# Kernel optimization log

Measured on AMD Instinct MI355X. Metric: run time of the kernel, lower is better.

Reference implementation:

```python
import jax, jax.numpy as jnp
import numpy as np

B, S, D, C = 8, 4096, 512, 2048


def setup_inputs() -> dict:
    key = jax.random.key(0)
    kx, kc = jax.random.split(key)
    x = jax.random.normal(kx, (B, S, D), dtype=jnp.float32)
    # kaiming_uniform_(a=sqrt(5)) on a [*,D,C] tensor ~ U(-bound, bound); exact init
    # distribution is irrelevant for the math, so plain scaled uniform is used.
    bound = 1.0 / np.sqrt(D)
    codebook = jax.random.uniform(kc, (1, 1, D, C), dtype=jnp.float32,
                                  minval=-bound, maxval=bound)
    return {"x": x, "codebook": codebook}


def reference(x, codebook):
    # Original: ((x[..., :, None] - codebook) ** 2).mean(dim=-2) -> [B, S, C]
    # Equivalent GEMM form: mean_d(x_d^2) + mean_d(c_dk^2) - (2/D) * x . c_k
    d = x.shape[-1]
    cb = codebook.reshape(codebook.shape[-2], codebook.shape[-1])  # [D, C]
    x2 = jnp.mean(x * x, axis=-1, keepdims=True)                   # [B, S, 1]
    c2 = jnp.mean(cb * cb, axis=0)                                 # [C]
    xc = jnp.einsum('bsd,dc->bsc', x, cb) / d                      # [B, S, C]
    return x2 + c2 - 2.0 * xc
```

## Files before the change

kernel.cpp:

```cpp
#include <hip/hip_runtime.h>
#include <hip/hip_bf16.h>


typedef __attribute__((ext_vector_type(8))) short bf16x8;
typedef __attribute__((ext_vector_type(4))) float f32x4;

#define M_ROWS 32768
#define K_DIM  512
#define N_COLS 2048

__device__ __forceinline__ unsigned short f2bf(float f) {
    unsigned int u = __float_as_uint(f);
    return (unsigned short)((u + 0x7fffu + ((u >> 16) & 1u)) >> 16);
}

__device__ __forceinline__ void gload_lds16(const void* g, void* l) {
    __builtin_amdgcn_global_load_lds(
        (const __attribute__((address_space(1))) unsigned int*)g,
        (__attribute__((address_space(3))) unsigned int*)l,
        16, 0, 0);
}

__global__ __launch_bounds__(256) void prep_x_kernel(const float* __restrict__ x,
                                                     unsigned short* __restrict__ xb,
                                                     float* __restrict__ x2) {
    const int wid = threadIdx.x >> 6;
    const int lane = threadIdx.x & 63;
    const int row = (blockIdx.x << 2) + wid;
    const float4* p4 = reinterpret_cast<const float4*>(x + (size_t)row * K_DIM);
    float4 v0 = p4[lane];
    float4 v1 = p4[lane + 64];
    float ss = v0.x*v0.x + v0.y*v0.y + v0.z*v0.z + v0.w*v0.w
             + v1.x*v1.x + v1.y*v1.y + v1.z*v1.z + v1.w*v1.w;
    union { unsigned short us[4]; uint2 u2; } pa, pb;
    pa.us[0] = f2bf(v0.x); pa.us[1] = f2bf(v0.y); pa.us[2] = f2bf(v0.z); pa.us[3] = f2bf(v0.w);
    pb.us[0] = f2bf(v1.x); pb.us[1] = f2bf(v1.y); pb.us[2] = f2bf(v1.z); pb.us[3] = f2bf(v1.w);
    uint2* dst = reinterpret_cast<uint2*>(xb + (size_t)row * K_DIM);
    dst[lane]      = pa.u2;
    dst[lane + 64] = pb.u2;
    #pragma unroll
    for (int off = 32; off; off >>= 1) ss += __shfl_xor(ss, off);
    if (lane == 0) x2[row] = ss * (1.0f / (float)K_DIM);
}

__global__ __launch_bounds__(256) void prep_cb_kernel(const float* __restrict__ cb,
                                                      unsigned short* __restrict__ cbT) {
    __shared__ float tile[32][65];
    const int k0 = blockIdx.x * 32;
    const int n0 = blockIdx.y * 64;
    const int tx = threadIdx.x & 63;
    const int ty = threadIdx.x >> 6;
    #pragma unroll
    for (int i = 0; i < 8; ++i) {
        const int k = ty + i * 4;
        tile[k][tx] = cb[(size_t)(k0 + k) * N_COLS + n0 + tx];
    }
    __syncthreads();
    const int kc = threadIdx.x & 31;
    const int nr = threadIdx.x >> 5;
    #pragma unroll
    for (int i = 0; i < 8; ++i) {
        const int n = nr + i * 8;
        cbT[(size_t)(n0 + n) * K_DIM + k0 + kc] = f2bf(tile[kc][n] * 0.00390625f);
    }
}

__global__ __launch_bounds__(256) void c2_kernel(const float* __restrict__ cb,
                                                 float* __restrict__ c2) {
    __shared__ float p[4][64];
    const int t = threadIdx.x;
    const int nl = t & 63;
    const int kc = t >> 6;
    const int n = blockIdx.x * 64 + nl;
    float s = 0.0f;
    for (int k = kc * 128; k < kc * 128 + 128; ++k) {
        float v = cb[(size_t)k * N_COLS + n];
        s += v * v;
    }
    p[kc][nl] = s;
    __syncthreads();
    if (t < 64) {
        c2[blockIdx.x * 64 + t] =
            (p[0][t] + p[1][t] + p[2][t] + p[3][t]) * (1.0f / (float)K_DIM);
    }
}


__device__ __forceinline__ bf16x8 frag_ld(const unsigned short* h, int r, int lhi) {
    const int off = r * 32 + ((lhi ^ ((r >> 1) & 3)) << 3);
    return *reinterpret_cast<const bf16x8*>(&h[off]);
}

#define BAR()  do { asm volatile("" ::: "memory"); \
                    __builtin_amdgcn_s_barrier();  \
                    asm volatile("" ::: "memory"); } while (0)
#define GATE_(n) asm volatile("s_waitcnt vmcnt(" #n ")" ::: "memory")
#define GATE(n) GATE_(n)

__global__ __launch_bounds__(512, 4) void gemm_kernel(
        const unsigned short* __restrict__ A,
        const unsigned short* __restrict__ Bt,
        const float* __restrict__ x2,
        const float* __restrict__ c2,
        float* __restrict__ out) {
    __shared__ unsigned short smem[3][12288];

    const int tid  = threadIdx.x;
    const int wid  = tid >> 6;
    const int lane = tid & 63;
    const int wr64 = (wid >> 2) * 64;
    const int wc64 = (wid & 3) * 64;
    const int l15 = lane & 15;
    const int lhi = lane >> 4;

    const int bid  = blockIdx.x;
    const int lbid = (bid & 7) * 256 + (bid >> 3);
    const int m0 = (lbid >> 3) * 128;
    const int n0 = (lbid & 7) * 256;

    const unsigned short* Ab = A  + (size_t)m0 * K_DIM;
    const unsigned short* Bb = Bt + (size_t)n0 * K_DIM;

    const int o16a  = wid * 64 + lane;
    const int rowa  = o16a >> 2;
    const int sla   = (o16a & 3) ^ ((rowa >> 1) & 3);
    const size_t aoff = (size_t)rowa * K_DIM + sla * 8;
    const int o16b0 = wid * 64 + lane;
    const int rowb0 = o16b0 >> 2;
    const size_t boff0 = (size_t)rowb0 * K_DIM + (((o16b0 & 3) ^ ((rowb0 >> 1) & 3)) * 8);
    const int o16b1 = 512 + wid * 64 + lane;
    const int rowb1 = o16b1 >> 2;
    const size_t boff1 = (size_t)rowb1 * K_DIM + (((o16b1 & 3) ^ ((rowb1 >> 1) & 3)) * 8);

    f32x4 acc[4][4] = {};

#define STAGE(KT, BUF)                                                         \
    do {                                                                       \
        gload_lds16(Ab + aoff  + (KT) * 32, &smem[(BUF)][wid * 512]);          \
        gload_lds16(Bb + boff0 + (KT) * 32, &smem[(BUF)][4096 + wid * 512]);   \
        gload_lds16(Bb + boff1 + (KT) * 32, &smem[(BUF)][8192 + wid * 512]);   \
    } while (0)

    STAGE(0, 0);
    STAGE(1, 1);
    GATE(3);
    BAR();

    #pragma unroll
    for (int t = 0; t < 16; ++t) {
        if (t < 14) STAGE(t + 2, (t + 2) % 3);
        const unsigned short* cbuf = smem[t % 3];
        bf16x8 a[4], b[4];
        #pragma unroll
        for (int mf = 0; mf < 4; ++mf)
            a[mf] = frag_ld(cbuf, wr64 + mf * 16 + l15, lhi);
        #pragma unroll
        for (int nf = 0; nf < 4; ++nf)
            b[nf] = frag_ld(cbuf + 4096, wc64 + nf * 16 + l15, lhi);
        __builtin_amdgcn_s_setprio(1);
        #pragma unroll
        for (int mf = 0; mf < 4; ++mf)
            #pragma unroll
            for (int nf = 0; nf < 4; ++nf)
                acc[mf][nf] = __builtin_amdgcn_mfma_f32_16x16x32_bf16(a[mf], b[nf], acc[mf][nf], 0, 0, 0);
        __builtin_amdgcn_s_setprio(0);
        if (t < 14) { GATE(3); } else if (t == 14) { GATE(0); }
        BAR();
    }
#undef STAGE

    #pragma unroll
    for (int mf = 0; mf < 4; ++mf) {
        const int mrow = m0 + wr64 + mf * 16 + lhi * 4;
        const float xv0 = x2[mrow + 0];
        const float xv1 = x2[mrow + 1];
        const float xv2 = x2[mrow + 2];
        const float xv3 = x2[mrow + 3];
        #pragma unroll
        for (int nf = 0; nf < 4; ++nf) {
            const int col = n0 + wc64 + nf * 16 + l15;
            const float cv = c2[col];
            float* o = out + (size_t)mrow * N_COLS + col;
            o[0 * N_COLS] = xv0 + cv - acc[mf][nf][0];
            o[1 * N_COLS] = xv1 + cv - acc[mf][nf][1];
            o[2 * N_COLS] = xv2 + cv - acc[mf][nf][2];
            o[3 * N_COLS] = xv3 + cv - acc[mf][nf][3];
        }
    }
}

extern "C" void kernel_launch(void* const* d_in, const int* in_sizes, int n_in,
                              void* d_out, int out_size, void* d_ws, size_t ws_size,
                              hipStream_t stream) {
    const float* x  = (const float*)d_in[0];
    const float* cb = (const float*)d_in[1];
    float* out = (float*)d_out;

    char* ws = (char*)d_ws;
    unsigned short* xb  = (unsigned short*)ws;
    unsigned short* cbT = (unsigned short*)(ws + (size_t)33554432);
    float* x2 = (float*)(ws + (size_t)33554432 + 2097152);
    float* c2 = (float*)(ws + (size_t)33554432 + 2097152 + 131072);

    prep_x_kernel<<<M_ROWS / 4, 256, 0, stream>>>(x, xb, x2);
    prep_cb_kernel<<<dim3(16, 32), 256, 0, stream>>>(cb, cbT);
    c2_kernel<<<N_COLS / 64, 256, 0, stream>>>(cb, c2);
    gemm_kernel<<<dim3((M_ROWS / 128) * (N_COLS / 256)), 512, 0, stream>>>(xb, cbT, x2, c2, out);
}
```

Baseline: 122.7 us.

## Fuse x bf16 conversion and row-norm into GEMM A-tile loading

Removes the separate prep_x kernel. The GEMM now loads fp32 x rows into registers, converts them to bf16 in-kernel and writes them into the swizzled LDS tile, accumulating the row sum of squares along the way. The row norms are reduced through shuffles into shared memory for the epilogue. This avoids writing and re-reading a 32MB bf16 copy plus a kernel launch. In exchange, each x row is re-read and re-converted by all 8 N-tile blocks, A global traffic per block doubles (fp32), and there is an extra register-staging wait in the pipeline.

```diff
diff --git a/kernel.cpp b/kernel.cpp
--- a/kernel.cpp
+++ b/kernel.cpp
@@ -19,28 +19,6 @@
         (const __attribute__((address_space(1))) unsigned int*)g,
         (__attribute__((address_space(3))) unsigned int*)l,
         16, 0, 0);
-}
-
-__global__ __launch_bounds__(256) void prep_x_kernel(const float* __restrict__ x,
-                                                     unsigned short* __restrict__ xb,
-                                                     float* __restrict__ x2) {
-    const int wid = threadIdx.x >> 6;
-    const int lane = threadIdx.x & 63;
-    const int row = (blockIdx.x << 2) + wid;
-    const float4* p4 = reinterpret_cast<const float4*>(x + (size_t)row * K_DIM);
-    float4 v0 = p4[lane];
-    float4 v1 = p4[lane + 64];
-    float ss = v0.x*v0.x + v0.y*v0.y + v0.z*v0.z + v0.w*v0.w
-             + v1.x*v1.x + v1.y*v1.y + v1.z*v1.z + v1.w*v1.w;
-    union { unsigned short us[4]; uint2 u2; } pa, pb;
-    pa.us[0] = f2bf(v0.x); pa.us[1] = f2bf(v0.y); pa.us[2] = f2bf(v0.z); pa.us[3] = f2bf(v0.w);
-    pb.us[0] = f2bf(v1.x); pb.us[1] = f2bf(v1.y); pb.us[2] = f2bf(v1.z); pb.us[3] = f2bf(v1.w);
-    uint2* dst = reinterpret_cast<uint2*>(xb + (size_t)row * K_DIM);
-    dst[lane]      = pa.u2;
-    dst[lane + 64] = pb.u2;
-    #pragma unroll
-    for (int off = 32; off; off >>= 1) ss += __shfl_xor(ss, off);
-    if (lane == 0) x2[row] = ss * (1.0f / (float)K_DIM);
 }
 
 __global__ __launch_bounds__(256) void prep_cb_kernel(const float* __restrict__ cb,
@@ -96,14 +74,15 @@
                     asm volatile("" ::: "memory"); } while (0)
 #define GATE_(n) asm volatile("s_waitcnt vmcnt(" #n ")" ::: "memory")
 #define GATE(n) GATE_(n)
+#define LGKM0() asm volatile("s_waitcnt lgkmcnt(0)" ::: "memory")
 
 __global__ __launch_bounds__(512, 4) void gemm_kernel(
-        const unsigned short* __restrict__ A,
+        const float* __restrict__ X,
         const unsigned short* __restrict__ Bt,
-        const float* __restrict__ x2,
         const float* __restrict__ c2,
         float* __restrict__ out) {
     __shared__ unsigned short smem[3][12288];
+    __shared__ float x2s[128];
 
     const int tid  = threadIdx.x;
     const int wid  = tid >> 6;
@@ -118,13 +97,13 @@
     const int m0 = (lbid >> 3) * 128;
     const int n0 = (lbid & 7) * 256;
 
-    const unsigned short* Ab = A  + (size_t)m0 * K_DIM;
+    const int arow = tid >> 2;
+    const int aq   = tid & 3;
+    const int asl  = aq ^ ((arow >> 1) & 3);
+    const int awchunk = (arow * 4 + asl) * 8;
+    const float* Ab = X + (size_t)(m0 + arow) * K_DIM + aq * 8;
+
     const unsigned short* Bb = Bt + (size_t)n0 * K_DIM;
-
-    const int o16a  = wid * 64 + lane;
-    const int rowa  = o16a >> 2;
-    const int sla   = (o16a & 3) ^ ((rowa >> 1) & 3);
-    const size_t aoff = (size_t)rowa * K_DIM + sla * 8;
     const int o16b0 = wid * 64 + lane;
     const int rowb0 = o16b0 >> 2;
     const size_t boff0 = (size_t)rowb0 * K_DIM + (((o16b0 & 3) ^ ((rowb0 >> 1) & 3)) * 8);
@@ -133,22 +112,41 @@
     const size_t boff1 = (size_t)rowb1 * K_DIM + (((o16b1 & 3) ^ ((rowb1 >> 1) & 3)) * 8);
 
     f32x4 acc[4][4] = {};
-
-#define STAGE(KT, BUF)                                                         \
-    do {                                                                       \
-        gload_lds16(Ab + aoff  + (KT) * 32, &smem[(BUF)][wid * 512]);          \
-        gload_lds16(Bb + boff0 + (KT) * 32, &smem[(BUF)][4096 + wid * 512]);   \
-        gload_lds16(Bb + boff1 + (KT) * 32, &smem[(BUF)][8192 + wid * 512]);   \
-    } while (0)
-
-    STAGE(0, 0);
-    STAGE(1, 1);
-    GATE(3);
+    float4 rA[2][2];
+    float ss = 0.0f;
+
+#define AISSUE(KT, P) do {                                                     \
+    const float4* p_ = reinterpret_cast<const float4*>(Ab + (KT) * 32);        \
+    rA[P][0] = p_[0]; rA[P][1] = p_[1]; } while (0)
+
+#define BISSUE(KT, BUF) do {                                                   \
+    gload_lds16(Bb + boff0 + (KT) * 32, &smem[(BUF)][4096 + wid * 512]);       \
+    gload_lds16(Bb + boff1 + (KT) * 32, &smem[(BUF)][8192 + wid * 512]); } while (0)
+
+#define AWRITE(BUF, P) do {                                                    \
+    union { unsigned short us[8]; bf16x8 v8; } u_;                             \
+    u_.us[0] = f2bf(rA[P][0].x); u_.us[1] = f2bf(rA[P][0].y);                  \
+    u_.us[2] = f2bf(rA[P][0].z); u_.us[3] = f2bf(rA[P][0].w);                  \
+    u_.us[4] = f2bf(rA[P][1].x); u_.us[5] = f2bf(rA[P][1].y);                  \
+    u_.us[6] = f2bf(rA[P][1].z); u_.us[7] = f2bf(rA[P][1].w);                  \
+    ss += rA[P][0].x * rA[P][0].x + rA[P][0].y * rA[P][0].y                    \
+        + rA[P][0].z * rA[P][0].z + rA[P][0].w * rA[P][0].w                    \
+        + rA[P][1].x * rA[P][1].x + rA[P][1].y * rA[P][1].y                    \
+        + rA[P][1].z * rA[P][1].z + rA[P][1].w * rA[P][1].w;                   \
+    *reinterpret_cast<bf16x8*>(&smem[(BUF)][awchunk]) = u_.v8; } while (0)
+
+    AISSUE(0, 0);
+    BISSUE(0, 0);
+    AISSUE(1, 1);
+    BISSUE(1, 1);
+    GATE(4);
+    AWRITE(0, 0);
+    LGKM0();
     BAR();
 
     #pragma unroll
     for (int t = 0; t < 16; ++t) {
-        if (t < 14) STAGE(t + 2, (t + 2) % 3);
+        if (t < 14) { AISSUE(t + 2, t & 1); BISSUE(t + 2, (t + 2) % 3); }
         const unsigned short* cbuf = smem[t % 3];
         bf16x8 a[4], b[4];
         #pragma unroll
@@ -164,18 +162,28 @@
             for (int nf = 0; nf < 4; ++nf)
                 acc[mf][nf] = __builtin_amdgcn_mfma_f32_16x16x32_bf16(a[mf], b[nf], acc[mf][nf], 0, 0, 0);
         __builtin_amdgcn_s_setprio(0);
-        if (t < 14) { GATE(3); } else if (t == 14) { GATE(0); }
+        if (t < 14) { GATE(4); } else if (t == 14) { GATE(0); }
+        if (t < 15) { AWRITE((t + 1) % 3, (t + 1) & 1); }
+        LGKM0();
         BAR();
     }
-#undef STAGE
+#undef AISSUE
+#undef BISSUE
+#undef AWRITE
+
+    ss += __shfl_xor(ss, 1);
+    ss += __shfl_xor(ss, 2);
+    if (aq == 0) x2s[arow] = ss * (1.0f / (float)K_DIM);
+    __syncthreads();
 
     #pragma unroll
     for (int mf = 0; mf < 4; ++mf) {
-        const int mrow = m0 + wr64 + mf * 16 + lhi * 4;
-        const float xv0 = x2[mrow + 0];
-        const float xv1 = x2[mrow + 1];
-        const float xv2 = x2[mrow + 2];
-        const float xv3 = x2[mrow + 3];
+        const int lrow = wr64 + mf * 16 + lhi * 4;
+        const int mrow = m0 + lrow;
+        const float xv0 = x2s[lrow + 0];
+        const float xv1 = x2s[lrow + 1];
+        const float xv2 = x2s[lrow + 2];
+        const float xv3 = x2s[lrow + 3];
         #pragma unroll
         for (int nf = 0; nf < 4; ++nf) {
             const int col = n0 + wc64 + nf * 16 + l15;
@@ -197,13 +205,10 @@
     float* out = (float*)d_out;
 
     char* ws = (char*)d_ws;
-    unsigned short* xb  = (unsigned short*)ws;
-    unsigned short* cbT = (unsigned short*)(ws + (size_t)33554432);
-    float* x2 = (float*)(ws + (size_t)33554432 + 2097152);
-    float* c2 = (float*)(ws + (size_t)33554432 + 2097152 + 131072);
-
-    prep_x_kernel<<<M_ROWS / 4, 256, 0, stream>>>(x, xb, x2);
+    unsigned short* cbT = (unsigned short*)ws;
+    float* c2 = (float*)(ws + (size_t)2097152);
+
     prep_cb_kernel<<<dim3(16, 32), 256, 0, stream>>>(cb, cbT);
     c2_kernel<<<N_COLS / 64, 256, 0, stream>>>(cb, c2);
-    gemm_kernel<<<dim3((M_ROWS / 128) * (N_COLS / 256)), 512, 0, stream>>>(xb, cbT, x2, c2, out);
-}
+    gemm_kernel<<<dim3((M_ROWS / 128) * (N_COLS / 256)), 512, 0, stream>>>(x, cbT, c2, out);
+}
```

After: 414.9 us. 3.38x slower.
